# Kernel optimization log

Measured on AMD Instinct MI355X. Metric: run time of the kernel, lower is better.

The kernel has to match this reference:

```python
import jax, jax.numpy as jnp
import numpy as np

N, E, F, H, L, G, C = 50000, 800000, 64, 128, 4, 64, 10
GAMMA = 10.0  # Gaussian RBF width for centers in (0,1)
CENTERS = jnp.linspace(0.0, 1.0, H)


def _ssp(v):
    # shifted softplus, SchNet's nonlinearity
    return jax.nn.softplus(v) - 0.6931472


def setup_inputs() -> dict:
    key = jax.random.key(0)
    ks = jax.random.split(key, 20)

    def w(k, shape, fan_in):
        return (jax.random.normal(k, shape, dtype=jnp.float32) / np.sqrt(fan_in)).astype(jnp.float32)

    x = jax.random.normal(ks[0], (N, F), dtype=jnp.float32)
    edge_dist = jax.random.uniform(ks[1], (E,), dtype=jnp.float32)
    edge_src = jax.random.randint(ks[2], (E,), 0, N, dtype=jnp.int32)
    edge_dst = jax.random.randint(ks[3], (E,), 0, N, dtype=jnp.int32)
    graph_ids = jnp.sort(jax.random.randint(ks[4], (N,), 0, G, dtype=jnp.int32))

    return {
        "x": x, "edge_dist": edge_dist,
        "edge_src": edge_src, "edge_dst": edge_dst, "graph_ids": graph_ids,
        # first-layer node projection F->H, remaining layers H->H (stacked)
        "W1_0": w(ks[5], (F, H), F), "b1_0": jnp.zeros((H,), jnp.float32),
        "W1_rest": w(ks[6], (L - 1, H, H), H), "b1_rest": jnp.zeros((L - 1, H), jnp.float32),
        # filter-generating MLP on RBF features, per layer
        "Wf1": w(ks[7], (L, H, H), H), "bf1": jnp.zeros((L, H), jnp.float32),
        "Wf2": w(ks[8], (L, H, H), H), "bf2": jnp.zeros((L, H), jnp.float32),
        # output projection per layer
        "W2": w(ks[9], (L, H, H), H), "b2": jnp.zeros((L, H), jnp.float32),
        # readout FC
        "fc_w": w(ks[10], (H, C), H), "fc_b": jnp.zeros((C,), jnp.float32),
    }


def _schnet_conv(x, rbf, src, dst, W1, b1, Wf1, bf1, Wf2, bf2, W2, b2):
    # CFConv: project nodes, gate gathered source features with a distance
    # filter, scatter-sum to destinations, project out.
    filt = _ssp(rbf @ Wf1 + bf1) @ Wf2 + bf2          # [E, H]
    h = x @ W1 + b1                                    # [N, H]
    msg = h[src] * filt                                # [E, H] gather + gate
    agg = jax.ops.segment_sum(msg, dst, num_segments=N)  # [N, H] scatter-sum
    return agg @ W2 + b2


def reference(x, edge_dist, edge_src, edge_dst, graph_ids,
              W1_0, b1_0, W1_rest, b1_rest, Wf1, bf1, Wf2, bf2, W2, b2,
              fc_w, fc_b):
    # Gaussian radial basis expansion of edge distances, shared across layers
    rbf = jnp.exp(-GAMMA * (edge_dist[:, None] - CENTERS) ** 2)  # [E, H]

    h = jax.nn.relu(_schnet_conv(x, rbf, edge_src, edge_dst,
                                 W1_0, b1_0, Wf1[0], bf1[0], Wf2[0], bf2[0],
                                 W2[0], b2[0]))
    for i in range(L - 1):
        h = jax.nn.relu(_schnet_conv(h, rbf, edge_src, edge_dst,
                                     W1_rest[i], b1_rest[i],
                                     Wf1[i + 1], bf1[i + 1],
                                     Wf2[i + 1], bf2[i + 1],
                                     W2[i + 1], b2[i + 1]))

    # dgl.mean_nodes: per-graph mean over nodes
    sums = jax.ops.segment_sum(h, graph_ids, num_segments=G)           # [G, H]
    cnts = jax.ops.segment_sum(jnp.ones((N,), h.dtype), graph_ids, num_segments=G)
    pooled = sums / jnp.maximum(cnts, 1.0)[:, None]

    logits = pooled @ fc_w + fc_b                                       # [G, C]
    return jax.nn.log_softmax(logits, axis=1)
```

## Files before the change

### kernel.cpp

```cpp
#include <hip/hip_runtime.h>
#include <math.h>

#define NN 50000
#define EE 800000
#define FF 64
#define HH 128
#define LL 4
#define GG 64
#define CC 10
#define TT 512
#define BD 64
#define ABLK 1024
#define EPB 782
#define SEGC 192
#define SUBB 96
#define SRW 6250

#define PB_CVTW 8
#define PB_TAB ((TT / 16) * LL)
#define PB_CVTX (NN * FF / 4 / 256)
#define PB_PART ABLK

typedef unsigned short ushort_t;
typedef unsigned int uint_t;

typedef short s8v __attribute__((ext_vector_type(8)));
typedef float f32x4 __attribute__((ext_vector_type(4)));

__device__ inline ushort_t f2bf(float f) {
  uint_t u = __float_as_uint(f);
  uint_t r = (u + 0x7FFFu + ((u >> 16) & 1u)) >> 16;
  return (ushort_t)r;
}
__device__ inline float bf_lo(uint_t pair) { return __uint_as_float(pair << 16); }
__device__ inline float bf_hi(uint_t pair) { return __uint_as_float(pair & 0xFFFF0000u); }
__device__ inline float bf1f(ushort_t v) { return __uint_as_float(((uint_t)v) << 16); }

__global__ __launch_bounds__(256) void prep(
    const float* __restrict__ x, ushort_t* __restrict__ xb,
    const float* __restrict__ W1_0, const float* __restrict__ W1_rest,
    const float* __restrict__ W2, ushort_t* __restrict__ wt,
    const float* __restrict__ Wf1, const float* __restrict__ bf1,
    const float* __restrict__ Wf2, const float* __restrict__ bf2,
    ushort_t* __restrict__ tables,
    const int* __restrict__ dst, const int* __restrict__ src,
    const float* __restrict__ dist,
    uint2* __restrict__ seg, int* __restrict__ segcnt, int* __restrict__ bcnt,
    const int* __restrict__ gid, int* __restrict__ gcnt, float* __restrict__ gsum) {
  __shared__ float rbf[16][HH];
  __shared__ float hid[16][HH];
  __shared__ int lcnt[8];
  int tid = threadIdx.x;
  int b = blockIdx.x;

  if (b < PB_CVTW) {
    int mid = b;
    const float* srcm; int K;
    if (mid == 0) { srcm = W1_0; K = FF; }
    else if (mid < 4) { srcm = W1_rest + (size_t)(mid - 1) * HH * HH; K = HH; }
    else { srcm = W2 + (size_t)(mid - 4) * HH * HH; K = HH; }
    ushort_t* dstm = wt + (size_t)mid * HH * HH;
    for (int idx = tid; idx < K * HH; idx += 256) {
      int k = idx >> 7, n = idx & 127;
      dstm[n * K + k] = f2bf(srcm[idx]);
    }
  } else if (b < PB_CVTW + PB_TAB) {
    int bb = b - PB_CVTW;
    int l = bb & 3;
    int tb = (bb >> 2) * 16;
    int j = tid & 127;
    float c = j * (1.0f / (HH - 1));
#pragma unroll
    for (int tt2 = 0; tt2 < 16; ++tt2) {
      float d = (tb + tt2) * (1.0f / (TT - 1));
      float dd = d - c;
      rbf[tt2][j] = expf(-10.0f * dd * dd);
    }
    __syncthreads();
    const float* W1f = Wf1 + (size_t)l * HH * HH;
    float s[16];
    float bb1 = bf1[l * HH + j];
#pragma unroll
    for (int tt2 = 0; tt2 < 16; ++tt2) s[tt2] = bb1;
    for (int k = 0; k < HH; ++k) {
      float wk = W1f[(size_t)k * HH + j];
#pragma unroll
      for (int tt2 = 0; tt2 < 16; ++tt2) s[tt2] += rbf[tt2][k] * wk;
    }
#pragma unroll
    for (int tt2 = 0; tt2 < 16; ++tt2)
      hid[tt2][j] = fmaxf(s[tt2], 0.f) + log1pf(expf(-fabsf(s[tt2]))) - 0.6931472f;
    __syncthreads();
    const float* W2f = Wf2 + (size_t)l * HH * HH;
    float bb2 = bf2[l * HH + j];
#pragma unroll
    for (int tt2 = 0; tt2 < 16; ++tt2) s[tt2] = bb2;
    for (int k = 0; k < HH; ++k) {
      float wk = W2f[(size_t)k * HH + j];
#pragma unroll
      for (int tt2 = 0; tt2 < 16; ++tt2) s[tt2] += hid[tt2][k] * wk;
    }
    if (tid < 128) {
#pragma unroll
      for (int tt2 = 0; tt2 < 16; ++tt2)
        tables[((size_t)l * TT + tb + tt2) * HH + j] = f2bf(s[tt2]);
    }
  } else if (b < PB_CVTW + PB_TAB + PB_CVTX) {
    int i = (b - PB_CVTW - PB_TAB) * 256 + tid;
    const float4* x4 = (const float4*)x;
    float4 v = x4[i];
    union { ushort_t us[4]; uint2 u; } pk;
    pk.us[0] = f2bf(v.x); pk.us[1] = f2bf(v.y); pk.us[2] = f2bf(v.z); pk.us[3] = f2bf(v.w);
    *(uint2*)&xb[i * 4] = pk.u;
  } else if (b < PB_CVTW + PB_TAB + PB_CVTX + PB_PART) {
    int pb = b - PB_CVTW - PB_TAB - PB_CVTX;
    if (tid < 8) lcnt[tid] = 0;
    int z = pb * 49 + tid;
    if (tid < 49 && z < NN) bcnt[z] = 0;
    __syncthreads();
    int e0 = pb * EPB;
    int e1 = min(e0 + EPB, EE);
    for (int e = e0 + tid; e < e1; e += 256) {
      int d = __builtin_nontemporal_load(dst + e);
      int s = __builtin_nontemporal_load(src + e);
      float di = __builtin_nontemporal_load(dist + e);
      float u = di * (float)(TT - 1);
      int t0 = (int)(fminf(fmaxf(u, 0.f), (float)(TT - 1)) + 0.5f);
      if (t0 > TT - 1) t0 = TT - 1;
      int r = d / SRW;
      int pos = atomicAdd(&lcnt[r], 1);
      if (pos < SEGC)
        seg[((size_t)(r << 10) + pb) * SEGC + pos] =
            make_uint2((uint_t)d, ((uint_t)s << 9) | (uint_t)t0);
    }
    __syncthreads();
    if (tid < 8) segcnt[(tid << 10) + pb] = min(lcnt[tid], SEGC);
  } else {
    for (int i = tid; i < GG * HH; i += 256) gsum[i] = 0.f;
    if (tid < GG) {
      int g = tid;
      int lo = 0, hi = NN;
      while (lo < hi) { int m = (lo + hi) >> 1; if (gid[m] < g) lo = m + 1; else hi = m; }
      int b0 = lo;
      lo = 0; hi = NN;
      int g1 = g + 1;
      while (lo < hi) { int m = (lo + hi) >> 1; if (gid[m] < g1) lo = m + 1; else hi = m; }
      gcnt[g] = lo - b0;
    }
  }
}

__global__ __launch_bounds__(256) void scatter_edges(
    const uint2* __restrict__ seg, const int* __restrict__ segcnt,
    int* __restrict__ bcnt, uint_t* __restrict__ epad) {
  int r = blockIdx.x & 7;
  int sub = blockIdx.x >> 3;
  int tid = threadIdx.x;
  for (int b = sub; b < ABLK; b += SUBB) {
    int cnt = segcnt[(r << 10) + b];
    const uint_t* sp = (const uint_t*)(seg + ((size_t)(r << 10) + b) * SEGC);
    for (int i = tid; i < cnt; i += 256) {
      uint_t ex = __builtin_nontemporal_load(sp + i * 2);
      uint_t ey = __builtin_nontemporal_load(sp + i * 2 + 1);
      int slot = atomicAdd(&bcnt[ex], 1);
      if (slot < BD) epad[(size_t)ex * BD + slot] = ey;
    }
  }
}

__global__ __launch_bounds__(256) void gemm_mfma(
    const ushort_t* __restrict__ A, const ushort_t* __restrict__ WT,
    const float* __restrict__ bias, ushort_t* __restrict__ OUT,
    int K, int act) {
  int lane = threadIdx.x & 63;
  int wave = threadIdx.x >> 6;
  int m = lane & 15;
  int quad = lane >> 4;
  int rowbase = blockIdx.x * 16;
  int colbase = wave * 32;
  const ushort_t* arow = A + (size_t)(rowbase + m) * K;
  const ushort_t* brow0 = WT + (size_t)(colbase + m) * K;
  const ushort_t* brow1 = WT + (size_t)(colbase + 16 + m) * K;
  f32x4 acc0 = {0.f, 0.f, 0.f, 0.f};
  f32x4 acc1 = {0.f, 0.f, 0.f, 0.f};
  for (int kc = 0; kc < K; kc += 32) {
    int k = kc + quad * 8;
    union { uint4 u; s8v v; } a, b0, b1;
    a.u  = *(const uint4*)(arow + k);
    b0.u = *(const uint4*)(brow0 + k);
    b1.u = *(const uint4*)(brow1 + k);
    acc0 = __builtin_amdgcn_mfma_f32_16x16x32_bf16(a.v, b0.v, acc0, 0, 0, 0);
    acc1 = __builtin_amdgcn_mfma_f32_16x16x32_bf16(a.v, b1.v, acc1, 0, 0, 0);
  }
  float bb0 = bias[colbase + m];
  float bb1 = bias[colbase + 16 + m];
#pragma unroll
  for (int reg = 0; reg < 4; ++reg) {
    int row = rowbase + quad * 4 + reg;
    float v0 = acc0[reg] + bb0;
    float v1 = acc1[reg] + bb1;
    if (act) { v0 = fmaxf(v0, 0.f); v1 = fmaxf(v1, 0.f); }
    OUT[(size_t)row * HH + colbase + m] = f2bf(v0);
    OUT[(size_t)row * HH + colbase + 16 + m] = f2bf(v1);
  }
}

__global__ __launch_bounds__(256) void gemm2_mfma(
    const ushort_t* __restrict__ AGG,
    const ushort_t* __restrict__ WT2, const float* __restrict__ b2l,
    const ushort_t* __restrict__ WT1, const float* __restrict__ b1l,
    ushort_t* __restrict__ OUT) {
  __shared__ ushort_t T[16 * 128];
  int lane = threadIdx.x & 63;
  int wave = threadIdx.x >> 6;
  int m = lane & 15;
  int quad = lane >> 4;
  int rowbase = blockIdx.x * 16;
  int colbase = wave * 32;
  {
    const ushort_t* arow = AGG + (size_t)(rowbase + m) * HH;
    const ushort_t* brow0 = WT2 + (size_t)(colbase + m) * HH;
    const ushort_t* brow1 = WT2 + (size_t)(colbase + 16 + m) * HH;
    f32x4 acc0 = {0.f, 0.f, 0.f, 0.f};
    f32x4 acc1 = {0.f, 0.f, 0.f, 0.f};
    for (int kc = 0; kc < HH; kc += 32) {
      int k = kc + quad * 8;
      union { uint4 u; s8v v; } a, b0, b1;
      a.u  = *(const uint4*)(arow + k);
      b0.u = *(const uint4*)(brow0 + k);
      b1.u = *(const uint4*)(brow1 + k);
      acc0 = __builtin_amdgcn_mfma_f32_16x16x32_bf16(a.v, b0.v, acc0, 0, 0, 0);
      acc1 = __builtin_amdgcn_mfma_f32_16x16x32_bf16(a.v, b1.v, acc1, 0, 0, 0);
    }
    float bb0 = b2l[colbase + m];
    float bb1 = b2l[colbase + 16 + m];
#pragma unroll
    for (int reg = 0; reg < 4; ++reg) {
      int r = quad * 4 + reg;
      float v0 = fmaxf(acc0[reg] + bb0, 0.f);
      float v1 = fmaxf(acc1[reg] + bb1, 0.f);
      int c0 = colbase + m, c1 = colbase + 16 + m;
      T[r * 128 + (((c0 >> 3) ^ r) << 3) + (c0 & 7)] = f2bf(v0);
      T[r * 128 + (((c1 >> 3) ^ r) << 3) + (c1 & 7)] = f2bf(v1);
    }
  }
  __syncthreads();
  {
    const ushort_t* brow0 = WT1 + (size_t)(colbase + m) * HH;
    const ushort_t* brow1 = WT1 + (size_t)(colbase + 16 + m) * HH;
    f32x4 acc0 = {0.f, 0.f, 0.f, 0.f};
    f32x4 acc1 = {0.f, 0.f, 0.f, 0.f};
    for (int kc = 0; kc < HH; kc += 32) {
      int k0 = kc + quad * 8;
      int g = k0 >> 3;
      union { uint4 u; s8v v; } a, b0, b1;
      a.u = *(const uint4*)&T[m * 128 + ((g ^ m) << 3)];
      b0.u = *(const uint4*)(brow0 + k0);
      b1.u = *(const uint4*)(brow1 + k0);
      acc0 = __builtin_amdgcn_mfma_f32_16x16x32_bf16(a.v, b0.v, acc0, 0, 0, 0);
      acc1 = __builtin_amdgcn_mfma_f32_16x16x32_bf16(a.v, b1.v, acc1, 0, 0, 0);
    }
    float bb0 = b1l[colbase + m];
    float bb1 = b1l[colbase + 16 + m];
#pragma unroll
    for (int reg = 0; reg < 4; ++reg) {
      int row = rowbase + quad * 4 + reg;
      OUT[(size_t)row * HH + colbase + m] = f2bf(acc0[reg] + bb0);
      OUT[(size_t)row * HH + colbase + 16 + m] = f2bf(acc1[reg] + bb1);
    }
  }
}

__global__ __launch_bounds__(256) void edge_agg(
    const ushort_t* __restrict__ p, const ushort_t* __restrict__ table,
    const uint_t* __restrict__ epad, const int* __restrict__ bcnt,
    ushort_t* __restrict__ agg) {
  int v = (blockIdx.x << 2) + (threadIdx.x >> 6);
  int lane = threadIdx.x & 63;
  if (v >= NN) return;
  int n = min(bcnt[v], BD);
  uint_t ed = (lane < n) ? epad[(size_t)v * BD + lane] : 0u;
  float ax = 0.f, ay = 0.f;
  int i = 0;
  int n4 = n & ~3;
  for (; i < n4; i += 4) {
    uint_t e0 = __shfl(ed, i + 0), e1 = __shfl(ed, i + 1);
    uint_t e2 = __shfl(ed, i + 2), e3 = __shfl(ed, i + 3);
    const uint_t* P0 = (const uint_t*)(p + (size_t)(e0 >> 9) * HH);
    const uint_t* P1 = (const uint_t*)(p + (size_t)(e1 >> 9) * HH);
    const uint_t* P2 = (const uint_t*)(p + (size_t)(e2 >> 9) * HH);
    const uint_t* P3 = (const uint_t*)(p + (size_t)(e3 >> 9) * HH);
    const uint_t* T0 = (const uint_t*)(table + (size_t)(e0 & 511u) * HH);
    const uint_t* T1 = (const uint_t*)(table + (size_t)(e1 & 511u) * HH);
    const uint_t* T2 = (const uint_t*)(table + (size_t)(e2 & 511u) * HH);
    const uint_t* T3 = (const uint_t*)(table + (size_t)(e3 & 511u) * HH);
    uint_t pv0 = P0[lane], pv1 = P1[lane], pv2 = P2[lane], pv3 = P3[lane];
    uint_t f0 = T0[lane], f1 = T1[lane], f2 = T2[lane], f3 = T3[lane];
    ax += bf_lo(pv0) * bf_lo(f0); ay += bf_hi(pv0) * bf_hi(f0);
    ax += bf_lo(pv1) * bf_lo(f1); ay += bf_hi(pv1) * bf_hi(f1);
    ax += bf_lo(pv2) * bf_lo(f2); ay += bf_hi(pv2) * bf_hi(f2);
    ax += bf_lo(pv3) * bf_lo(f3); ay += bf_hi(pv3) * bf_hi(f3);
  }
  for (; i < n; ++i) {
    uint_t e = __shfl(ed, i);
    uint_t pv = ((const uint_t*)(p + (size_t)(e >> 9) * HH))[lane];
    uint_t f = ((const uint_t*)(table + (size_t)(e & 511u) * HH))[lane];
    ax += bf_lo(pv) * bf_lo(f);
    ay += bf_hi(pv) * bf_hi(f);
  }
  uint_t packed = (uint_t)f2bf(ax) | ((uint_t)f2bf(ay) << 16);
  ((uint_t*)agg)[(size_t)v * 64 + lane] = packed;
}

__global__ __launch_bounds__(128) void pool_kernel(const ushort_t* __restrict__ h, const int* __restrict__ gid,
                                                   float* __restrict__ gsum) {
  int j = threadIdx.x;
  int i0 = blockIdx.x * 128;
  int i1 = min(i0 + 128, NN);
  if (i0 >= NN) return;
  float acc = 0.f;
  int gcur = gid[i0];
  for (int i = i0; i < i1; ++i) {
    int g = gid[i];
    if (g != gcur) {
      atomicAdd(&gsum[gcur * HH + j], acc);
      acc = 0.f;
      gcur = g;
    }
    acc += bf1f(h[(size_t)i * HH + j]);
  }
  atomicAdd(&gsum[gcur * HH + j], acc);
}

__global__ __launch_bounds__(128) void final_kernel(const float* __restrict__ gsum, const int* __restrict__ gcnt,
                                                    const float* __restrict__ fc_w, const float* __restrict__ fc_b,
                                                    float* __restrict__ out) {
  int g = blockIdx.x, j = threadIdx.x;
  __shared__ float pooled[HH];
  __shared__ float logits[CC];
  __shared__ float lse;
  float cnt = fmaxf((float)gcnt[g], 1.0f);
  pooled[j] = gsum[g * HH + j] / cnt;
  __syncthreads();
  if (j < CC) {
    float s = fc_b[j];
    for (int k = 0; k < HH; ++k) s += pooled[k] * fc_w[k * CC + j];
    logits[j] = s;
  }
  __syncthreads();
  if (j == 0) {
    float m = -1e30f;
    for (int c = 0; c < CC; ++c) m = fmaxf(m, logits[c]);
    float s = 0.f;
    for (int c = 0; c < CC; ++c) s += expf(logits[c] - m);
    lse = m + logf(s);
  }
  __syncthreads();
  if (j < CC) out[g * CC + j] = logits[j] - lse;
}

extern "C" void kernel_launch(void* const* d_in, const int* in_sizes, int n_in,
                              void* d_out, int out_size, void* d_ws, size_t ws_size,
                              hipStream_t stream) {
  const float* x       = (const float*)d_in[0];
  const float* edist   = (const float*)d_in[1];
  const int*   esrc    = (const int*)d_in[2];
  const int*   edst    = (const int*)d_in[3];
  const int*   gid     = (const int*)d_in[4];
  const float* W1_0    = (const float*)d_in[5];
  const float* b1_0    = (const float*)d_in[6];
  const float* W1_rest = (const float*)d_in[7];
  const float* b1_rest = (const float*)d_in[8];
  const float* Wf1     = (const float*)d_in[9];
  const float* bf1     = (const float*)d_in[10];
  const float* Wf2     = (const float*)d_in[11];
  const float* bf2     = (const float*)d_in[12];
  const float* W2      = (const float*)d_in[13];
  const float* b2      = (const float*)d_in[14];
  const float* fc_w    = (const float*)d_in[15];
  const float* fc_b    = (const float*)d_in[16];
  float* out = (float*)d_out;

  char* ws = (char*)d_ws;
  size_t o = 0;
  auto alloc = [&](size_t bytes) {
    void* p = ws + o;
    o += (bytes + 255) & ~(size_t)255;
    return p;
  };
  ushort_t* tables = (ushort_t*)alloc(sizeof(ushort_t) * (size_t)LL * TT * HH);
  ushort_t* xb     = (ushort_t*)alloc(sizeof(ushort_t) * (size_t)NN * FF);
  ushort_t* wt     = (ushort_t*)alloc(sizeof(ushort_t) * 8 * HH * HH);
  ushort_t* pbuf   = (ushort_t*)alloc(sizeof(ushort_t) * (size_t)NN * HH);
  ushort_t* hbuf   = (ushort_t*)alloc(sizeof(ushort_t) * (size_t)NN * HH);
  ushort_t* aggbuf = (ushort_t*)alloc(sizeof(ushort_t) * (size_t)NN * HH);
  int*      bcnt   = (int*)alloc(sizeof(int) * NN);
  uint_t*   epad   = (uint_t*)alloc(sizeof(uint_t) * (size_t)NN * BD);
  uint2*    seg    = (uint2*)alloc(sizeof(uint2) * (size_t)8 * ABLK * SEGC);
  int*      segcnt = (int*)alloc(sizeof(int) * 8 * ABLK);
  float*    gsum   = (float*)alloc(sizeof(float) * GG * HH);
  int*      gcnt   = (int*)alloc(sizeof(int) * GG);

  const int prepBlocks = PB_CVTW + PB_TAB + PB_CVTX + PB_PART + 1;
  prep<<<prepBlocks, 256, 0, stream>>>(x, xb, W1_0, W1_rest, W2, wt,
                                       Wf1, bf1, Wf2, bf2, tables,
                                       edst, esrc, edist, seg, segcnt, bcnt,
                                       gid, gcnt, gsum);
  scatter_edges<<<8 * SUBB, 256, 0, stream>>>(seg, segcnt, bcnt, epad);

  const int gemmBlocks = NN / 16;
  gemm_mfma<<<gemmBlocks, 256, 0, stream>>>(xb, wt, b1_0, pbuf, FF, 0);
  for (int l = 0; l < LL; ++l) {
    edge_agg<<<(NN + 3) / 4, 256, 0, stream>>>(pbuf, tables + (size_t)l * TT * HH,
                                               epad, bcnt, aggbuf);
    if (l < LL - 1) {
      gemm2_mfma<<<gemmBlocks, 256, 0, stream>>>(aggbuf,
                                                 wt + (size_t)(4 + l) * HH * HH, b2 + (size_t)l * HH,
                                                 wt + (size_t)(1 + l) * HH * HH, b1_rest + (size_t)l * HH,
                                                 pbuf);
    } else {
      gemm_mfma<<<gemmBlocks, 256, 0, stream>>>(aggbuf, wt + (size_t)(4 + l) * HH * HH,
                                                b2 + (size_t)l * HH, hbuf, HH, 1);
    }
  }

  pool_kernel<<<(NN + 127) / 128, 128, 0, stream>>>(hbuf, gid, gsum);
  final_kernel<<<GG, 128, 0, stream>>>(gsum, gcnt, fc_w, fc_b, out);
}
```

Measured before the change: 463.3 us.

## Fuse edge aggregation with output GEMMs and merge scatter, first GEMM, pooling kernels

```diff
diff --git a/kernel.cpp b/kernel.cpp
--- a/kernel.cpp
+++ b/kernel.cpp
@@ -21,6 +21,9 @@
 #define PB_CVTX (NN * FF / 4 / 256)
 #define PB_PART ABLK
 
+#define SCB (8 * SUBB)
+#define GEMMB (NN / 16)
+
 typedef unsigned short ushort_t;
 typedef unsigned int uint_t;
 
@@ -46,7 +49,7 @@
     const int* __restrict__ dst, const int* __restrict__ src,
     const float* __restrict__ dist,
     uint2* __restrict__ seg, int* __restrict__ segcnt, int* __restrict__ bcnt,
-    const int* __restrict__ gid, int* __restrict__ gcnt, float* __restrict__ gsum) {
+    const int* __restrict__ gid, int* __restrict__ gcnt) {
   __shared__ float rbf[16][HH];
   __shared__ float hid[16][HH];
   __shared__ int lcnt[8];
@@ -136,7 +139,6 @@
     __syncthreads();
     if (tid < 8) segcnt[(tid << 10) + pb] = min(lcnt[tid], SEGC);
   } else {
-    for (int i = tid; i < GG * HH; i += 256) gsum[i] = 0.f;
     if (tid < GG) {
       int g = tid;
       int lo = 0, hi = NN;
@@ -150,80 +152,35 @@
   }
 }
 
-__global__ __launch_bounds__(256) void scatter_edges(
+__global__ __launch_bounds__(256) void scatter_gemm1(
     const uint2* __restrict__ seg, const int* __restrict__ segcnt,
-    int* __restrict__ bcnt, uint_t* __restrict__ epad) {
-  int r = blockIdx.x & 7;
-  int sub = blockIdx.x >> 3;
+    int* __restrict__ bcnt, uint_t* __restrict__ epad,
+    const ushort_t* __restrict__ xb, const ushort_t* __restrict__ wt,
+    const float* __restrict__ b1_0, ushort_t* __restrict__ pbuf) {
   int tid = threadIdx.x;
-  for (int b = sub; b < ABLK; b += SUBB) {
-    int cnt = segcnt[(r << 10) + b];
-    const uint_t* sp = (const uint_t*)(seg + ((size_t)(r << 10) + b) * SEGC);
-    for (int i = tid; i < cnt; i += 256) {
-      uint_t ex = __builtin_nontemporal_load(sp + i * 2);
-      uint_t ey = __builtin_nontemporal_load(sp + i * 2 + 1);
-      int slot = atomicAdd(&bcnt[ex], 1);
-      if (slot < BD) epad[(size_t)ex * BD + slot] = ey;
-    }
-  }
-}
-
-__global__ __launch_bounds__(256) void gemm_mfma(
-    const ushort_t* __restrict__ A, const ushort_t* __restrict__ WT,
-    const float* __restrict__ bias, ushort_t* __restrict__ OUT,
-    int K, int act) {
-  int lane = threadIdx.x & 63;
-  int wave = threadIdx.x >> 6;
-  int m = lane & 15;
-  int quad = lane >> 4;
-  int rowbase = blockIdx.x * 16;
-  int colbase = wave * 32;
-  const ushort_t* arow = A + (size_t)(rowbase + m) * K;
-  const ushort_t* brow0 = WT + (size_t)(colbase + m) * K;
-  const ushort_t* brow1 = WT + (size_t)(colbase + 16 + m) * K;
-  f32x4 acc0 = {0.f, 0.f, 0.f, 0.f};
-  f32x4 acc1 = {0.f, 0.f, 0.f, 0.f};
-  for (int kc = 0; kc < K; kc += 32) {
-    int k = kc + quad * 8;
-    union { uint4 u; s8v v; } a, b0, b1;
-    a.u  = *(const uint4*)(arow + k);
-    b0.u = *(const uint4*)(brow0 + k);
-    b1.u = *(const uint4*)(brow1 + k);
-    acc0 = __builtin_amdgcn_mfma_f32_16x16x32_bf16(a.v, b0.v, acc0, 0, 0, 0);
-    acc1 = __builtin_amdgcn_mfma_f32_16x16x32_bf16(a.v, b1.v, acc1, 0, 0, 0);
-  }
-  float bb0 = bias[colbase + m];
-  float bb1 = bias[colbase + 16 + m];
-#pragma unroll
-  for (int reg = 0; reg < 4; ++reg) {
-    int row = rowbase + quad * 4 + reg;
-    float v0 = acc0[reg] + bb0;
-    float v1 = acc1[reg] + bb1;
-    if (act) { v0 = fmaxf(v0, 0.f); v1 = fmaxf(v1, 0.f); }
-    OUT[(size_t)row * HH + colbase + m] = f2bf(v0);
-    OUT[(size_t)row * HH + colbase + 16 + m] = f2bf(v1);
-  }
-}
-
-__global__ __launch_bounds__(256) void gemm2_mfma(
-    const ushort_t* __restrict__ AGG,
-    const ushort_t* __restrict__ WT2, const float* __restrict__ b2l,
-    const ushort_t* __restrict__ WT1, const float* __restrict__ b1l,
-    ushort_t* __restrict__ OUT) {
-  __shared__ ushort_t T[16 * 128];
-  int lane = threadIdx.x & 63;
-  int wave = threadIdx.x >> 6;
-  int m = lane & 15;
-  int quad = lane >> 4;
-  int rowbase = blockIdx.x * 16;
-  int colbase = wave * 32;
-  {
-    const ushort_t* arow = AGG + (size_t)(rowbase + m) * HH;
-    const ushort_t* brow0 = WT2 + (size_t)(colbase + m) * HH;
-    const ushort_t* brow1 = WT2 + (size_t)(colbase + 16 + m) * HH;
+  if (blockIdx.x < SCB) {
+    int r = blockIdx.x & 7;
+    int sub = blockIdx.x >> 3;
+    for (int b = sub; b < ABLK; b += SUBB) {
+      int cnt = segcnt[(r << 10) + b];
+      const uint_t* sp = (const uint_t*)(seg + ((size_t)(r << 10) + b) * SEGC);
+      for (int i = tid; i < cnt; i += 256) {
+        uint_t ex = __builtin_nontemporal_load(sp + i * 2);
+        uint_t ey = __builtin_nontemporal_load(sp + i * 2 + 1);
+        int slot = atomicAdd(&bcnt[ex], 1);
+        if (slot < BD) epad[(size_t)ex * BD + slot] = ey;
+      }
+    }
+  } else {
+    int tile = blockIdx.x - SCB;
+    int lane = tid & 63, wave = tid >> 6, m = lane & 15, quad = lane >> 4;
+    int rowbase = tile * 16, colbase = wave * 32;
+    const ushort_t* arow = xb + (size_t)(rowbase + m) * FF;
+    const ushort_t* brow0 = wt + (size_t)(colbase + m) * FF;
+    const ushort_t* brow1 = wt + (size_t)(colbase + 16 + m) * FF;
     f32x4 acc0 = {0.f, 0.f, 0.f, 0.f};
     f32x4 acc1 = {0.f, 0.f, 0.f, 0.f};
-    for (int kc = 0; kc < HH; kc += 32) {
+    for (int kc = 0; kc < FF; kc += 32) {
       int k = kc + quad * 8;
       union { uint4 u; s8v v; } a, b0, b1;
       a.u  = *(const uint4*)(arow + k);
@@ -232,8 +189,95 @@
       acc0 = __builtin_amdgcn_mfma_f32_16x16x32_bf16(a.v, b0.v, acc0, 0, 0, 0);
       acc1 = __builtin_amdgcn_mfma_f32_16x16x32_bf16(a.v, b1.v, acc1, 0, 0, 0);
     }
+    float bb0 = b1_0[colbase + m];
+    float bb1 = b1_0[colbase + 16 + m];
+#pragma unroll
+    for (int reg = 0; reg < 4; ++reg) {
+      int row = rowbase + quad * 4 + reg;
+      pbuf[(size_t)row * HH + colbase + m] = f2bf(acc0[reg] + bb0);
+      pbuf[(size_t)row * HH + colbase + 16 + m] = f2bf(acc1[reg] + bb1);
+    }
+  }
+}
+
+__global__ __launch_bounds__(256) void fused_layer(
+    const ushort_t* __restrict__ pIn, const ushort_t* __restrict__ table,
+    const uint_t* __restrict__ epad, const int* __restrict__ bcnt,
+    const ushort_t* __restrict__ WT2, const float* __restrict__ b2l,
+    const ushort_t* __restrict__ WT1, const float* __restrict__ b1l,
+    ushort_t* __restrict__ OUT, int last) {
+  __shared__ ushort_t At[16 * 128];
+  __shared__ ushort_t T[16 * 128];
+  int tid = threadIdx.x;
+  int lane = tid & 63;
+  int wv = tid >> 6;
+  int tile = blockIdx.x;
+#pragma unroll
+  for (int i = 0; i < 4; ++i) {
+    int r = wv * 4 + i;
+    int v = tile * 16 + r;
+    int n = min(bcnt[v], BD);
+    uint_t ed = (lane < n) ? epad[(size_t)v * BD + lane] : 0u;
+    float ax = 0.f, ay = 0.f;
+    int j = 0;
+    int n4 = n & ~3;
+    for (; j < n4; j += 4) {
+      uint_t e0 = __shfl(ed, j + 0), e1 = __shfl(ed, j + 1);
+      uint_t e2 = __shfl(ed, j + 2), e3 = __shfl(ed, j + 3);
+      const uint_t* P0 = (const uint_t*)(pIn + (size_t)(e0 >> 9) * HH);
+      const uint_t* P1 = (const uint_t*)(pIn + (size_t)(e1 >> 9) * HH);
+      const uint_t* P2 = (const uint_t*)(pIn + (size_t)(e2 >> 9) * HH);
+      const uint_t* P3 = (const uint_t*)(pIn + (size_t)(e3 >> 9) * HH);
+      const uint_t* T0 = (const uint_t*)(table + (size_t)(e0 & 511u) * HH);
+      const uint_t* T1 = (const uint_t*)(table + (size_t)(e1 & 511u) * HH);
+      const uint_t* T2 = (const uint_t*)(table + (size_t)(e2 & 511u) * HH);
+      const uint_t* T3 = (const uint_t*)(table + (size_t)(e3 & 511u) * HH);
+      uint_t pv0 = P0[lane], pv1 = P1[lane], pv2 = P2[lane], pv3 = P3[lane];
+      uint_t f0 = T0[lane], f1 = T1[lane], f2 = T2[lane], f3 = T3[lane];
+      ax += bf_lo(pv0) * bf_lo(f0); ay += bf_hi(pv0) * bf_hi(f0);
+      ax += bf_lo(pv1) * bf_lo(f1); ay += bf_hi(pv1) * bf_hi(f1);
+      ax += bf_lo(pv2) * bf_lo(f2); ay += bf_hi(pv2) * bf_hi(f2);
+      ax += bf_lo(pv3) * bf_lo(f3); ay += bf_hi(pv3) * bf_hi(f3);
+    }
+    for (; j < n; ++j) {
+      uint_t e = __shfl(ed, j);
+      uint_t pv = ((const uint_t*)(pIn + (size_t)(e >> 9) * HH))[lane];
+      uint_t f = ((const uint_t*)(table + (size_t)(e & 511u) * HH))[lane];
+      ax += bf_lo(pv) * bf_lo(f);
+      ay += bf_hi(pv) * bf_hi(f);
+    }
+    uint_t packed = (uint_t)f2bf(ax) | ((uint_t)f2bf(ay) << 16);
+    ((uint_t*)At)[r * 64 + (((lane >> 2) ^ r) << 2) + (lane & 3)] = packed;
+  }
+  __syncthreads();
+  int m = lane & 15, quad = lane >> 4;
+  int rowbase = tile * 16, colbase = wv * 32;
+  {
+    const ushort_t* brow0 = WT2 + (size_t)(colbase + m) * HH;
+    const ushort_t* brow1 = WT2 + (size_t)(colbase + 16 + m) * HH;
+    f32x4 acc0 = {0.f, 0.f, 0.f, 0.f};
+    f32x4 acc1 = {0.f, 0.f, 0.f, 0.f};
+    for (int kc = 0; kc < HH; kc += 32) {
+      int k = kc + quad * 8;
+      int g = k >> 3;
+      union { uint4 u; s8v v; } a, b0, b1;
+      a.u = *(const uint4*)&At[m * 128 + ((g ^ m) << 3)];
+      b0.u = *(const uint4*)(brow0 + k);
+      b1.u = *(const uint4*)(brow1 + k);
+      acc0 = __builtin_amdgcn_mfma_f32_16x16x32_bf16(a.v, b0.v, acc0, 0, 0, 0);
+      acc1 = __builtin_amdgcn_mfma_f32_16x16x32_bf16(a.v, b1.v, acc1, 0, 0, 0);
+    }
     float bb0 = b2l[colbase + m];
     float bb1 = b2l[colbase + 16 + m];
+    if (last) {
+#pragma unroll
+      for (int reg = 0; reg < 4; ++reg) {
+        int row = rowbase + quad * 4 + reg;
+        OUT[(size_t)row * HH + colbase + m] = f2bf(fmaxf(acc0[reg] + bb0, 0.f));
+        OUT[(size_t)row * HH + colbase + 16 + m] = f2bf(fmaxf(acc1[reg] + bb1, 0.f));
+      }
+      return;
+    }
 #pragma unroll
     for (int reg = 0; reg < 4; ++reg) {
       int r = quad * 4 + reg;
@@ -271,76 +315,23 @@
   }
 }
 
-__global__ __launch_bounds__(256) void edge_agg(
-    const ushort_t* __restrict__ p, const ushort_t* __restrict__ table,
-    const uint_t* __restrict__ epad, const int* __restrict__ bcnt,
-    ushort_t* __restrict__ agg) {
-  int v = (blockIdx.x << 2) + (threadIdx.x >> 6);
-  int lane = threadIdx.x & 63;
-  if (v >= NN) return;
-  int n = min(bcnt[v], BD);
-  uint_t ed = (lane < n) ? epad[(size_t)v * BD + lane] : 0u;
-  float ax = 0.f, ay = 0.f;
-  int i = 0;
-  int n4 = n & ~3;
-  for (; i < n4; i += 4) {
-    uint_t e0 = __shfl(ed, i + 0), e1 = __shfl(ed, i + 1);
-    uint_t e2 = __shfl(ed, i + 2), e3 = __shfl(ed, i + 3);
-    const uint_t* P0 = (const uint_t*)(p + (size_t)(e0 >> 9) * HH);
-    const uint_t* P1 = (const uint_t*)(p + (size_t)(e1 >> 9) * HH);
-    const uint_t* P2 = (const uint_t*)(p + (size_t)(e2 >> 9) * HH);
-    const uint_t* P3 = (const uint_t*)(p + (size_t)(e3 >> 9) * HH);
-    const uint_t* T0 = (const uint_t*)(table + (size_t)(e0 & 511u) * HH);
-    const uint_t* T1 = (const uint_t*)(table + (size_t)(e1 & 511u) * HH);
-    const uint_t* T2 = (const uint_t*)(table + (size_t)(e2 & 511u) * HH);
-    const uint_t* T3 = (const uint_t*)(table + (size_t)(e3 & 511u) * HH);
-    uint_t pv0 = P0[lane], pv1 = P1[lane], pv2 = P2[lane], pv3 = P3[lane];
-    uint_t f0 = T0[lane], f1 = T1[lane], f2 = T2[lane], f3 = T3[lane];
-    ax += bf_lo(pv0) * bf_lo(f0); ay += bf_hi(pv0) * bf_hi(f0);
-    ax += bf_lo(pv1) * bf_lo(f1); ay += bf_hi(pv1) * bf_hi(f1);
-    ax += bf_lo(pv2) * bf_lo(f2); ay += bf_hi(pv2) * bf_hi(f2);
-    ax += bf_lo(pv3) * bf_lo(f3); ay += bf_hi(pv3) * bf_hi(f3);
-  }
-  for (; i < n; ++i) {
-    uint_t e = __shfl(ed, i);
-    uint_t pv = ((const uint_t*)(p + (size_t)(e >> 9) * HH))[lane];
-    uint_t f = ((const uint_t*)(table + (size_t)(e & 511u) * HH))[lane];
-    ax += bf_lo(pv) * bf_lo(f);
-    ay += bf_hi(pv) * bf_hi(f);
-  }
-  uint_t packed = (uint_t)f2bf(ax) | ((uint_t)f2bf(ay) << 16);
-  ((uint_t*)agg)[(size_t)v * 64 + lane] = packed;
-}
-
-__global__ __launch_bounds__(128) void pool_kernel(const ushort_t* __restrict__ h, const int* __restrict__ gid,
-                                                   float* __restrict__ gsum) {
-  int j = threadIdx.x;
-  int i0 = blockIdx.x * 128;
-  int i1 = min(i0 + 128, NN);
-  if (i0 >= NN) return;
-  float acc = 0.f;
-  int gcur = gid[i0];
-  for (int i = i0; i < i1; ++i) {
-    int g = gid[i];
-    if (g != gcur) {
-      atomicAdd(&gsum[gcur * HH + j], acc);
-      acc = 0.f;
-      gcur = g;
-    }
-    acc += bf1f(h[(size_t)i * HH + j]);
-  }
-  atomicAdd(&gsum[gcur * HH + j], acc);
-}
-
-__global__ __launch_bounds__(128) void final_kernel(const float* __restrict__ gsum, const int* __restrict__ gcnt,
-                                                    const float* __restrict__ fc_w, const float* __restrict__ fc_b,
-                                                    float* __restrict__ out) {
-  int g = blockIdx.x, j = threadIdx.x;
+__global__ __launch_bounds__(128) void poolfinal(
+    const ushort_t* __restrict__ h, const int* __restrict__ gid,
+    const int* __restrict__ gcnt,
+    const float* __restrict__ fc_w, const float* __restrict__ fc_b,
+    float* __restrict__ out) {
   __shared__ float pooled[HH];
   __shared__ float logits[CC];
   __shared__ float lse;
-  float cnt = fmaxf((float)gcnt[g], 1.0f);
-  pooled[j] = gsum[g * HH + j] / cnt;
+  int g = blockIdx.x, j = threadIdx.x;
+  int lo = 0, hi = NN;
+  while (lo < hi) { int m = (lo + hi) >> 1; if (gid[m] < g) lo = m + 1; else hi = m; }
+  int b0 = lo;
+  int cnt = gcnt[g];
+  int b1 = b0 + cnt;
+  float acc = 0.f;
+  for (int i = b0; i < b1; ++i) acc += bf1f(h[(size_t)i * HH + j]);
+  pooled[j] = acc / fmaxf((float)cnt, 1.0f);
   __syncthreads();
   if (j < CC) {
     float s = fc_b[j];
@@ -349,11 +340,11 @@
   }
   __syncthreads();
   if (j == 0) {
-    float m = -1e30f;
-    for (int c = 0; c < CC; ++c) m = fmaxf(m, logits[c]);
+    float mx = -1e30f;
+    for (int c = 0; c < CC; ++c) mx = fmaxf(mx, logits[c]);
     float s = 0.f;
-    for (int c = 0; c < CC; ++c) s += expf(logits[c] - m);
-    lse = m + logf(s);
+    for (int c = 0; c < CC; ++c) s += expf(logits[c] - mx);
+    lse = mx + logf(s);
   }
   __syncthreads();
   if (j < CC) out[g * CC + j] = logits[j] - lse;
@@ -392,38 +383,34 @@
   ushort_t* xb     = (ushort_t*)alloc(sizeof(ushort_t) * (size_t)NN * FF);
   ushort_t* wt     = (ushort_t*)alloc(sizeof(ushort_t) * 8 * HH * HH);
   ushort_t* pbuf   = (ushort_t*)alloc(sizeof(ushort_t) * (size_t)NN * HH);
+  ushort_t* pbuf2  = (ushort_t*)alloc(sizeof(ushort_t) * (size_t)NN * HH);
   ushort_t* hbuf   = (ushort_t*)alloc(sizeof(ushort_t) * (size_t)NN * HH);
-  ushort_t* aggbuf = (ushort_t*)alloc(sizeof(ushort_t) * (size_t)NN * HH);
   int*      bcnt   = (int*)alloc(sizeof(int) * NN);
   uint_t*   epad   = (uint_t*)alloc(sizeof(uint_t) * (size_t)NN * BD);
   uint2*    seg    = (uint2*)alloc(sizeof(uint2) * (size_t)8 * ABLK * SEGC);
   int*      segcnt = (int*)alloc(sizeof(int) * 8 * ABLK);
-  float*    gsum   = (float*)alloc(sizeof(float) * GG * HH);
   int*      gcnt   = (int*)alloc(sizeof(int) * GG);
 
   const int prepBlocks = PB_CVTW + PB_TAB + PB_CVTX + PB_PART + 1;
   prep<<<prepBlocks, 256, 0, stream>>>(x, xb, W1_0, W1_rest, W2, wt,
                                        Wf1, bf1, Wf2, bf2, tables,
                                        edst, esrc, edist, seg, segcnt, bcnt,
-                                       gid, gcnt, gsum);
-  scatter_edges<<<8 * SUBB, 256, 0, stream>>>(seg, segcnt, bcnt, epad);
-
-  const int gemmBlocks = NN / 16;
-  gemm_mfma<<<gemmBlocks, 256, 0, stream>>>(xb, wt, b1_0, pbuf, FF, 0);
+                                       gid, gcnt);
+  scatter_gemm1<<<SCB + GEMMB, 256, 0, stream>>>(seg, segcnt, bcnt, epad,
+                                                 xb, wt, b1_0, pbuf);
+
+  ushort_t* pIn = pbuf;
+  ushort_t* pOut = pbuf2;
   for (int l = 0; l < LL; ++l) {
-    edge_agg<<<(NN + 3) / 4, 256, 0, stream>>>(pbuf, tables + (size_t)l * TT * HH,
-                                               epad, bcnt, aggbuf);
-    if (l < LL - 1) {
-      gemm2_mfma<<<gemmBlocks, 256, 0, stream>>>(aggbuf,
-                                                 wt + (size_t)(4 + l) * HH * HH, b2 + (size_t)l * HH,
-                                                 wt + (size_t)(1 + l) * HH * HH, b1_rest + (size_t)l * HH,
-                                                 pbuf);
-    } else {
-      gemm_mfma<<<gemmBlocks, 256, 0, stream>>>(aggbuf, wt + (size_t)(4 + l) * HH * HH,
-                                                b2 + (size_t)l * HH, hbuf, HH, 1);
-    }
-  }
-
-  pool_kernel<<<(NN + 127) / 128, 128, 0, stream>>>(hbuf, gid, gsum);
-  final_kernel<<<GG, 128, 0, stream>>>(gsum, gcnt, fc_w, fc_b, out);
-}
+    int last = (l == LL - 1);
+    fused_layer<<<GEMMB, 256, 0, stream>>>(
+        pIn, tables + (size_t)l * TT * HH, epad, bcnt,
+        wt + (size_t)(4 + l) * HH * HH, b2 + (size_t)l * HH,
+        last ? nullptr : (wt + (size_t)(1 + l) * HH * HH),
+        last ? nullptr : (b1_rest + (size_t)l * HH),
+        last ? hbuf : pOut, last);
+    ushort_t* tmp = pIn; pIn = pOut; pOut = tmp;
+  }
+
+  poolfinal<<<GG, 128, 0, stream>>>(hbuf, gid, gcnt, fc_w, fc_b, out);
+}
```

Measured after the change: 571.2 us. 1.23x slower.
